# Kernel optimization log

Measured on AMD Instinct MI355X. Metric: run time of the kernel, lower is better.

## Reference

```python
import jax, jax.numpy as jnp
import numpy as np

N = 100_000      # nodes
F_IN = 512       # input feature dim
HID = 8          # hidden per head (layer 1)
HEADS = 8        # heads layer 1
CLS = 7          # num classes (layer 2 out, 1 head)
E = 1_600_000    # random edges (self-loops added in reference)
NEG_SLOPE = 0.2  # PyG GATConv default leaky_relu slope


def setup_inputs() -> dict:
    key = jax.random.key(0)
    ks = jax.random.split(key, 10)
    s1 = 1.0 / np.sqrt(F_IN)
    s2 = 1.0 / np.sqrt(HID * HEADS)
    return {
        "x": jax.random.normal(ks[0], (N, F_IN), jnp.float32),
        "edge_index": jax.random.randint(ks[1], (2, E), 0, N, dtype=jnp.int32),
        "W1": jax.random.normal(ks[2], (F_IN, HEADS * HID), jnp.float32) * s1,
        "a_src1": jax.random.normal(ks[3], (HEADS, HID), jnp.float32) * s1,
        "a_dst1": jax.random.normal(ks[4], (HEADS, HID), jnp.float32) * s1,
        "b1": jnp.zeros((HEADS * HID,), jnp.float32),
        "W2": jax.random.normal(ks[5], (HEADS * HID, CLS), jnp.float32) * s2,
        "a_src2": jax.random.normal(ks[6], (1, CLS), jnp.float32) * s2,
        "a_dst2": jax.random.normal(ks[7], (1, CLS), jnp.float32) * s2,
        "b2": jnp.zeros((CLS,), jnp.float32),
    }


def gat_layer(x, edge_index, W, a_src, a_dst, bias, concat):
    """PyG GATConv (eval mode): linear -> per-edge LeakyReLU score -> edge-softmax over
    incoming edges per dst node -> weighted scatter-sum of src messages."""
    n = x.shape[0]
    H, C = a_src.shape
    h = (x @ W).reshape(n, H, C)                      # [N, H, C]
    src, dst = edge_index[0], edge_index[1]
    alpha_src = (h * a_src).sum(-1)                   # [N, H]
    alpha_dst = (h * a_dst).sum(-1)                   # [N, H]
    e = jax.nn.leaky_relu(alpha_src[src] + alpha_dst[dst], NEG_SLOPE)  # [E, H]
    # numerically stable segment softmax over edges grouped by dst
    m = jax.ops.segment_max(e, dst, num_segments=n)   # [N, H]
    p = jnp.exp(e - m[dst])                           # [E, H]
    denom = jax.ops.segment_sum(p, dst, num_segments=n)
    alpha = p / denom[dst]                            # [E, H]
    out = jax.ops.segment_sum(alpha[:, :, None] * h[src], dst, num_segments=n)  # [N, H, C]
    out = out.reshape(n, H * C) if concat else out.mean(axis=1)
    return out + bias


def reference(x, edge_index, W1, a_src1, a_dst1, b1, W2, a_src2, a_dst2, b2):
    # add self-loops (GATConv default add_self_loops=True)
    loops = jnp.arange(N, dtype=edge_index.dtype)
    ei = jnp.concatenate([edge_index, jnp.stack([loops, loops])], axis=1)
    h = jax.nn.elu(gat_layer(x, ei, W1, a_src1, a_dst1, b1, concat=True))
    out = gat_layer(h, ei, W2, a_src2, a_dst2, b2, concat=False)
    return jax.nn.log_softmax(out, axis=1)
```

## Files before the change

kernel.cpp:

```cpp
#include <hip/hip_runtime.h>
#include <hip/hip_bf16.h>

#define NEG_SLOPE 0.2f
#define SB 256
#define HWG 384

typedef __attribute__((ext_vector_type(8))) short bfrag;
typedef __attribute__((ext_vector_type(4))) float f32x4;
typedef unsigned short ushort_t;

__device__ __forceinline__ float lrelu(float x) {
    return x >= 0.0f ? x : NEG_SLOPE * x;
}
__device__ __forceinline__ unsigned short f2bf(float f) {
    unsigned int u = __float_as_uint(f);
    u += 0x7fffu + ((u >> 16) & 1u);
    return (unsigned short)(u >> 16);
}
__device__ __forceinline__ float bf2f(unsigned short h) {
    return __uint_as_float(((unsigned int)h) << 16);
}
__device__ __forceinline__ float u2lo(unsigned int u) {
    return __uint_as_float(u << 16);
}
__device__ __forceinline__ float u2hi(unsigned int u) {
    return __uint_as_float(u & 0xffff0000u);
}

__global__ __launch_bounds__(256) void hist_prep_kernel(
    const int* __restrict__ edst, int* __restrict__ bcnt, int E, int NB,
    const float* __restrict__ W1, ushort_t* __restrict__ Whi,
    ushort_t* __restrict__ Wlo) {
    if (blockIdx.x < 128) {
        int t = blockIdx.x * 256 + threadIdx.x;
        int k = t >> 6, c = t & 63;
        float w = W1[t];
        unsigned short hi = f2bf(w);
        float rem = w - bf2f(hi);
        int dst = (k >> 7) * 8192 + c * 128 + (k & 127);
        Whi[dst] = hi;
        Wlo[dst] = f2bf(rem);
        return;
    }
    __shared__ int hist[512];
    int tid = threadIdx.x;
    for (int i = tid; i < NB; i += 256) hist[i] = 0;
    __syncthreads();
    int wg = blockIdx.x - 128;
    int CH = (E + HWG - 1) / HWG;
    int st = wg * CH, en = min(st + CH, E);
    for (int i = st + tid; i < en; i += 256)
        atomicAdd(&hist[edst[i] >> 8], 1);
    __syncthreads();
    for (int i = tid; i < NB; i += 256)
        if (hist[i] > 0) atomicAdd(&bcnt[i], hist[i]);
}

__global__ __launch_bounds__(512) void bscan_kernel(
    const int* __restrict__ bcnt, int* __restrict__ boff, int* __restrict__ bcur,
    int* __restrict__ csr_off, int NB, int N, int E) {
    __shared__ int s[512];
    int t = threadIdx.x;
    int v = (t < NB) ? bcnt[t] : 0;
    s[t] = v;
    __syncthreads();
    for (int off = 1; off < 512; off <<= 1) {
        int tv = (t >= off) ? s[t - off] : 0;
        __syncthreads();
        s[t] += tv;
        __syncthreads();
    }
    if (t < NB) {
        int o = s[t] - v;
        boff[t] = o;
        bcur[t] = o;
    }
    if (t == 0) {
        boff[NB] = E;
        csr_off[N] = E;
    }
}

__global__ __launch_bounds__(256) void gemm_bscatter_kernel(
    const float* __restrict__ x, const ushort_t* __restrict__ Whi,
    const ushort_t* __restrict__ Wlo, ushort_t* __restrict__ h1b, int n,
    const int* __restrict__ esrc, const int* __restrict__ edst,
    int* __restrict__ bcur, int2* __restrict__ ebuf, int E, int NB) {
    __shared__ __align__(16) ushort_t Bhi[64 * 136];
    __shared__ __align__(16) ushort_t Blo[64 * 136];
    const int tid = threadIdx.x;

    if (blockIdx.x < SB) {
        int* hist = (int*)Bhi;
        int* base = hist + 512;
        int* rank = hist + 1024;
        for (int i = tid; i < NB; i += 256) { hist[i] = 0; rank[i] = 0; }
        __syncthreads();
        int CH = (E + SB - 1) / SB;
        int st = blockIdx.x * CH, en = min(st + CH, E);
        for (int i = st + tid; i < en; i += 256)
            atomicAdd(&hist[edst[i] >> 8], 1);
        __syncthreads();
        for (int b = tid; b < NB; b += 256)
            if (hist[b] > 0) base[b] = atomicAdd(&bcur[b], hist[b]);
        __syncthreads();
        for (int i = st + tid; i < en; i += 256) {
            int d = edst[i], s = esrc[i];
            int b = d >> 8;
            int r = atomicAdd(&rank[b], 1);
            ebuf[base[b] + r] = make_int2(s, d);
        }
        return;
    }

    const int lane = tid & 63;
    const int wave = tid >> 6;
    const int l15 = lane & 15;
    const int lq = lane >> 4;
    const int wb = (blockIdx.x - SB) * 64 + wave * 16;

    f32x4 acc[4];
    #pragma unroll
    for (int t = 0; t < 4; t++) acc[t] = (f32x4){0.f, 0.f, 0.f, 0.f};

    const int arow = min(wb + l15, n - 1);
    const float* xr = x + (size_t)arow * 512;

    for (int p = 0; p < 4; p++) {
        __syncthreads();
        const ushort_t* sh = Whi + p * 8192;
        const ushort_t* sl = Wlo + p * 8192;
        #pragma unroll
        for (int i = 0; i < 4; i++) {
            int lin = (tid + i * 256) * 8;
            int c = lin >> 7, kk = lin & 127;
            *(bfrag*)&Bhi[c * 136 + kk] = *(const bfrag*)&sh[lin];
            *(bfrag*)&Blo[c * 136 + kk] = *(const bfrag*)&sl[lin];
        }
        __syncthreads();

        #pragma unroll
        for (int step = 0; step < 4; step++) {
            int kb = p * 128 + step * 32 + lq * 8;
            float4 v0 = *(const float4*)&xr[kb];
            float4 v1 = *(const float4*)&xr[kb + 4];
            float xf[8] = {v0.x, v0.y, v0.z, v0.w, v1.x, v1.y, v1.z, v1.w};
            bfrag ah, al;
            #pragma unroll
            for (int j = 0; j < 8; j++) {
                unsigned short hi = f2bf(xf[j]);
                float rem = xf[j] - bf2f(hi);
                ah[j] = (short)hi;
                al[j] = (short)f2bf(rem);
            }
            int kloc = step * 32 + lq * 8;
            #pragma unroll
            for (int t = 0; t < 4; t++) {
                int nrow = t * 16 + l15;
                bfrag bh = *(const bfrag*)&Bhi[nrow * 136 + kloc];
                bfrag bl = *(const bfrag*)&Blo[nrow * 136 + kloc];
                acc[t] = __builtin_amdgcn_mfma_f32_16x16x32_bf16(al, bh, acc[t], 0, 0, 0);
                acc[t] = __builtin_amdgcn_mfma_f32_16x16x32_bf16(ah, bl, acc[t], 0, 0, 0);
                acc[t] = __builtin_amdgcn_mfma_f32_16x16x32_bf16(ah, bh, acc[t], 0, 0, 0);
            }
        }
    }
    #pragma unroll
    for (int t = 0; t < 4; t++) {
        #pragma unroll
        for (int reg = 0; reg < 4; reg++) {
            int grow = wb + lq * 4 + reg;
            if (grow < n) h1b[(size_t)grow * 64 + t * 16 + l15] = f2bf(acc[t][reg]);
        }
    }
}

__global__ __launch_bounds__(256) void finalize_as_kernel(
    const int* __restrict__ boff, const int2* __restrict__ ebuf,
    int* __restrict__ csr_off, int* __restrict__ col, int N, int NB,
    const ushort_t* __restrict__ h1b, const float* __restrict__ a_src1,
    const float* __restrict__ a_dst1, float* __restrict__ as1,
    float* __restrict__ ad1) {
    int tid = threadIdx.x;
    if ((int)blockIdx.x < NB) {
        int b = blockIdx.x;
        __shared__ int cnt[256];
        __shared__ int cur[256];
        __shared__ int sc[256];
        cnt[tid] = 0;
        __syncthreads();
        int st = boff[b], en = boff[b + 1];
        for (int i = st + tid; i < en; i += 256)
            atomicAdd(&cnt[ebuf[i].y & 255], 1);
        __syncthreads();
        int v = cnt[tid];
        sc[tid] = v;
        __syncthreads();
        for (int off = 1; off < 256; off <<= 1) {
            int tv = (tid >= off) ? sc[tid - off] : 0;
            __syncthreads();
            sc[tid] += tv;
            __syncthreads();
        }
        int dbase = b << 8;
        int nd = min(256, N - dbase);
        int o = st + sc[tid] - v;
        if (tid < nd) {
            csr_off[dbase + tid] = o;
            cur[tid] = o;
        }
        __syncthreads();
        for (int i = st + tid; i < en; i += 256) {
            int2 p = ebuf[i];
            int r = atomicAdd(&cur[p.y & 255], 1);
            col[r] = p.x;
        }
        return;
    }
    int idx = ((int)blockIdx.x - NB) * 256 + tid;
    if (idx >= N * 8) return;
    int h = idx & 7;
    const ushort_t* row = h1b + (size_t)(idx >> 3) * 64;
    bfrag hv = *(const bfrag*)&row[h * 8];
    float s = 0.f, d = 0.f;
    #pragma unroll
    for (int j = 0; j < 8; j++) {
        float f = bf2f((unsigned short)hv[j]);
        s = fmaf(f, a_src1[h * 8 + j], s);
        d = fmaf(f, a_dst1[h * 8 + j], d);
    }
    as1[idx] = s;
    ad1[idx] = d;
}

__global__ __launch_bounds__(256) void agg1_kernel(
    const int* __restrict__ csr_off, const int* __restrict__ col,
    const ushort_t* __restrict__ h1b, const float* __restrict__ as1,
    const float* __restrict__ ad1,
    const float* __restrict__ b1, const float* __restrict__ W2,
    const float* __restrict__ a_src2, const float* __restrict__ a_dst2,
    float* __restrict__ g2, float* __restrict__ ad2, int n) {
    int d = blockIdx.x * 8 + (threadIdx.x >> 5);
    if (d >= n) return;
    int c = threadIdx.x & 31;
    int hd = c >> 2;
    const ushort_t* myrow = h1b + (size_t)d * 64;
    float adh = ad1[d * 8 + hd];
    float asd = as1[d * 8 + hd];
    float p0 = __expf(lrelu(asd + adh));
    unsigned int u = *(const unsigned int*)(myrow + c * 2);
    float denom = p0;
    float acc0 = p0 * u2lo(u);
    float acc1 = p0 * u2hi(u);
    int st = csr_off[d], en = csr_off[d + 1];
    int e = st;
    for (; e + 2 <= en; e += 2) {
        int s0 = col[e], s1 = col[e + 1];
        const ushort_t* r0 = h1b + (size_t)s0 * 64;
        const ushort_t* r1 = h1b + (size_t)s1 * 64;
        float a0 = as1[s0 * 8 + hd];
        float a1 = as1[s1 * 8 + hd];
        unsigned int u0 = *(const unsigned int*)(r0 + c * 2);
        unsigned int u1 = *(const unsigned int*)(r1 + c * 2);
        float q0 = __expf(lrelu(a0 + adh));
        float q1 = __expf(lrelu(a1 + adh));
        denom += q0 + q1;
        acc0 = fmaf(q0, u2lo(u0), acc0);
        acc1 = fmaf(q0, u2hi(u0), acc1);
        acc0 = fmaf(q1, u2lo(u1), acc0);
        acc1 = fmaf(q1, u2hi(u1), acc1);
    }
    if (e < en) {
        int s0 = col[e];
        const ushort_t* r0 = h1b + (size_t)s0 * 64;
        float a0 = as1[s0 * 8 + hd];
        unsigned int u0 = *(const unsigned int*)(r0 + c * 2);
        float q0 = __expf(lrelu(a0 + adh));
        denom += q0;
        acc0 = fmaf(q0, u2lo(u0), acc0);
        acc1 = fmaf(q0, u2hi(u0), acc1);
    }
    float v0 = acc0 / denom + b1[2 * c];
    float v1 = acc1 / denom + b1[2 * c + 1];
    float h0 = v0 > 0.f ? v0 : (__expf(v0) - 1.f);
    float h1v = v1 > 0.f ? v1 : (__expf(v1) - 1.f);
    float g[7];
    #pragma unroll
    for (int j = 0; j < 7; j++) {
        float t = fmaf(h0, W2[(2 * c) * 7 + j], h1v * W2[(2 * c + 1) * 7 + j]);
        #pragma unroll
        for (int off = 1; off < 32; off <<= 1) t += __shfl_xor(t, off);
        g[j] = t;
    }
    float sa = 0.f, da = 0.f;
    #pragma unroll
    for (int j = 0; j < 7; j++) {
        sa = fmaf(g[j], a_src2[j], sa);
        da = fmaf(g[j], a_dst2[j], da);
    }
    if (c < 7) g2[(size_t)d * 8 + c] = g[c];
    if (c == 7) g2[(size_t)d * 8 + 7] = sa;
    if (c == 8) ad2[d] = da;
}

__global__ __launch_bounds__(256) void agg2_kernel(
    const int* __restrict__ csr_off, const int* __restrict__ col,
    const float* __restrict__ ad2, const float* __restrict__ g2,
    const float* __restrict__ b2, float* __restrict__ out, int n) {
    int d = blockIdx.x * 4 + (threadIdx.x >> 6);
    if (d >= n) return;
    int lane = threadIdx.x & 63;
    int j = lane >> 3, cc = lane & 7;
    int bl = lane | 7;
    float adv = ad2[d];
    float vd = g2[(size_t)d * 8 + cc];
    float as2d = __shfl(vd, bl);
    float pd = (j == 0) ? __expf(lrelu(as2d + adv)) : 0.f;
    float denom = pd;
    float acc = pd * vd;
    int st = csr_off[d], en = csr_off[d + 1];
    for (int base = st; base < en; base += 8) {
        int eidx = base + j;
        bool valid = eidx < en;
        int s = valid ? col[eidx] : d;
        float val = g2[(size_t)s * 8 + cc];
        float as2s = __shfl(val, bl);
        float p = valid ? __expf(lrelu(as2s + adv)) : 0.f;
        denom += p;
        acc = fmaf(p, val, acc);
    }
    #pragma unroll
    for (int off = 8; off < 64; off <<= 1) {
        acc += __shfl_xor(acc, off);
        denom += __shfl_xor(denom, off);
    }
    float o = acc / denom + ((cc < 7) ? b2[cc] : 0.f);
    float m = (cc < 7) ? o : -1e30f;
    #pragma unroll
    for (int off = 1; off < 8; off <<= 1) m = fmaxf(m, __shfl_xor(m, off));
    float se = (cc < 7) ? __expf(o - m) : 0.f;
    #pragma unroll
    for (int off = 1; off < 8; off <<= 1) se += __shfl_xor(se, off);
    float lse = m + __logf(se);
    if (j == 0 && cc < 7) out[(size_t)d * 7 + cc] = o - lse;
}

extern "C" void kernel_launch(void* const* d_in, const int* in_sizes, int n_in,
                              void* d_out, int out_size, void* d_ws, size_t ws_size,
                              hipStream_t stream) {
    const float* x      = (const float*)d_in[0];
    const int*   ei     = (const int*)d_in[1];
    const float* W1     = (const float*)d_in[2];
    const float* a_src1 = (const float*)d_in[3];
    const float* a_dst1 = (const float*)d_in[4];
    const float* b1     = (const float*)d_in[5];
    const float* W2     = (const float*)d_in[6];
    const float* a_src2 = (const float*)d_in[7];
    const float* a_dst2 = (const float*)d_in[8];
    const float* b2     = (const float*)d_in[9];

    int N = in_sizes[0] / 512;
    int E = in_sizes[1] / 2;
    const int* esrc = ei;
    const int* edst = ei + E;
    int NB = (N + 255) >> 8;

    char* ws = (char*)d_ws;
    size_t off = 0;
    auto alloc = [&](size_t bytes) -> void* {
        void* p = ws + off;
        off += (bytes + 255) & ~(size_t)255;
        return p;
    };
    ushort_t* h1b  = (ushort_t*)alloc((size_t)N * 64 * 2);
    float* as1     = (float*)alloc((size_t)N * 8 * 4);
    float* ad1     = (float*)alloc((size_t)N * 8 * 4);
    float* g2      = (float*)alloc((size_t)N * 8 * 4);
    float* ad2     = (float*)alloc((size_t)N * 4);
    int*   csr_off = (int*)alloc((size_t)(N + 1) * 4);
    int*   col     = (int*)alloc((size_t)E * 4);
    int2*  ebuf    = (int2*)alloc((size_t)E * 8);
    ushort_t* Whi  = (ushort_t*)alloc(512 * 64 * 2);
    ushort_t* Wlo  = (ushort_t*)alloc(512 * 64 * 2);
    int*   bcnt    = (int*)alloc((size_t)NB * 4);
    int*   boff    = (int*)alloc((size_t)(NB + 1) * 4);
    int*   bcur    = (int*)alloc((size_t)NB * 4);

    hipMemsetAsync(bcnt, 0, (size_t)NB * 4, stream);

    int gbl = (N + 63) / 64;
    int abl = (N * 8 + 255) / 256;

    hist_prep_kernel<<<128 + HWG, 256, 0, stream>>>(edst, bcnt, E, NB, W1, Whi, Wlo);
    bscan_kernel<<<1, 512, 0, stream>>>(bcnt, boff, bcur, csr_off, NB, N, E);
    gemm_bscatter_kernel<<<SB + gbl, 256, 0, stream>>>(x, Whi, Wlo, h1b, N,
                                                       esrc, edst, bcur, ebuf, E, NB);
    finalize_as_kernel<<<NB + abl, 256, 0, stream>>>(boff, ebuf, csr_off, col, N, NB,
                                                     h1b, a_src1, a_dst1, as1, ad1);
    agg1_kernel<<<(N + 7) / 8, 256, 0, stream>>>(csr_off, col, h1b, as1, ad1, b1,
                                                 W2, a_src2, a_dst2, g2, ad2, N);
    agg2_kernel<<<(N + 3) / 4, 256, 0, stream>>>(csr_off, col, ad2, g2, b2,
                                                 (float*)d_out, N);
}
```

Before: 479.8 us.

## Fuse attention score projection into GEMM epilogue and unroll agg1 edge loop by four

Computes the per-head alpha_src/alpha_dst dot products directly from the fp32 MFMA accumulators in the GEMM epilogue, using cross-lane shuffles. This removes the separate pass that re-read h1b from memory in the finalize kernel, which now only builds the CSR. The scores now come from fp32 accumulators instead of bf16-rounded values, which changes numerics slightly. The agg1 neighbour loop is also unrolled from 2 to 4 edges so more gather loads are in flight at once, at the cost of extra registers.

```diff
diff --git a/kernel.cpp b/kernel.cpp
--- a/kernel.cpp
+++ b/kernel.cpp
@@ -85,7 +85,9 @@
     const float* __restrict__ x, const ushort_t* __restrict__ Whi,
     const ushort_t* __restrict__ Wlo, ushort_t* __restrict__ h1b, int n,
     const int* __restrict__ esrc, const int* __restrict__ edst,
-    int* __restrict__ bcur, int2* __restrict__ ebuf, int E, int NB) {
+    int* __restrict__ bcur, int2* __restrict__ ebuf, int E, int NB,
+    const float* __restrict__ a_src1, const float* __restrict__ a_dst1,
+    float* __restrict__ as1, float* __restrict__ ad1) {
     __shared__ __align__(16) ushort_t Bhi[64 * 136];
     __shared__ __align__(16) ushort_t Blo[64 * 136];
     const int tid = threadIdx.x;
@@ -173,64 +175,77 @@
             if (grow < n) h1b[(size_t)grow * 64 + t * 16 + l15] = f2bf(acc[t][reg]);
         }
     }
-}
-
-__global__ __launch_bounds__(256) void finalize_as_kernel(
+    const int j7 = l15 & 7;
+    const int wrow = wb + lq * 4 + (j7 & 3);
+    #pragma unroll
+    for (int t = 0; t < 4; t++) {
+        int cidx = t * 16 + l15;
+        float cs = a_src1[cidx];
+        float cd = a_dst1[cidx];
+        float ps0 = acc[t][0] * cs, ps1 = acc[t][1] * cs;
+        float ps2 = acc[t][2] * cs, ps3 = acc[t][3] * cs;
+        float pd0 = acc[t][0] * cd, pd1 = acc[t][1] * cd;
+        float pd2 = acc[t][2] * cd, pd3 = acc[t][3] * cd;
+        #pragma unroll
+        for (int off = 1; off < 8; off <<= 1) {
+            ps0 += __shfl_xor(ps0, off);
+            ps1 += __shfl_xor(ps1, off);
+            ps2 += __shfl_xor(ps2, off);
+            ps3 += __shfl_xor(ps3, off);
+            pd0 += __shfl_xor(pd0, off);
+            pd1 += __shfl_xor(pd1, off);
+            pd2 += __shfl_xor(pd2, off);
+            pd3 += __shfl_xor(pd3, off);
+        }
+        int h = (t << 1) | (l15 >> 3);
+        if (wrow < n) {
+            if (j7 < 4) {
+                float sv = j7 == 0 ? ps0 : j7 == 1 ? ps1 : j7 == 2 ? ps2 : ps3;
+                as1[wrow * 8 + h] = sv;
+            } else {
+                float dv = j7 == 4 ? pd0 : j7 == 5 ? pd1 : j7 == 6 ? pd2 : pd3;
+                ad1[wrow * 8 + h] = dv;
+            }
+        }
+    }
+}
+
+__global__ __launch_bounds__(256) void finalize_kernel(
     const int* __restrict__ boff, const int2* __restrict__ ebuf,
-    int* __restrict__ csr_off, int* __restrict__ col, int N, int NB,
-    const ushort_t* __restrict__ h1b, const float* __restrict__ a_src1,
-    const float* __restrict__ a_dst1, float* __restrict__ as1,
-    float* __restrict__ ad1) {
+    int* __restrict__ csr_off, int* __restrict__ col, int N, int NB) {
     int tid = threadIdx.x;
-    if ((int)blockIdx.x < NB) {
-        int b = blockIdx.x;
-        __shared__ int cnt[256];
-        __shared__ int cur[256];
-        __shared__ int sc[256];
-        cnt[tid] = 0;
-        __syncthreads();
-        int st = boff[b], en = boff[b + 1];
-        for (int i = st + tid; i < en; i += 256)
-            atomicAdd(&cnt[ebuf[i].y & 255], 1);
-        __syncthreads();
-        int v = cnt[tid];
-        sc[tid] = v;
-        __syncthreads();
-        for (int off = 1; off < 256; off <<= 1) {
-            int tv = (tid >= off) ? sc[tid - off] : 0;
-            __syncthreads();
-            sc[tid] += tv;
-            __syncthreads();
-        }
-        int dbase = b << 8;
-        int nd = min(256, N - dbase);
-        int o = st + sc[tid] - v;
-        if (tid < nd) {
-            csr_off[dbase + tid] = o;
-            cur[tid] = o;
-        }
-        __syncthreads();
-        for (int i = st + tid; i < en; i += 256) {
-            int2 p = ebuf[i];
-            int r = atomicAdd(&cur[p.y & 255], 1);
-            col[r] = p.x;
-        }
-        return;
-    }
-    int idx = ((int)blockIdx.x - NB) * 256 + tid;
-    if (idx >= N * 8) return;
-    int h = idx & 7;
-    const ushort_t* row = h1b + (size_t)(idx >> 3) * 64;
-    bfrag hv = *(const bfrag*)&row[h * 8];
-    float s = 0.f, d = 0.f;
-    #pragma unroll
-    for (int j = 0; j < 8; j++) {
-        float f = bf2f((unsigned short)hv[j]);
-        s = fmaf(f, a_src1[h * 8 + j], s);
-        d = fmaf(f, a_dst1[h * 8 + j], d);
-    }
-    as1[idx] = s;
-    ad1[idx] = d;
+    int b = blockIdx.x;
+    __shared__ int cnt[256];
+    __shared__ int cur[256];
+    __shared__ int sc[256];
+    cnt[tid] = 0;
+    __syncthreads();
+    int st = boff[b], en = boff[b + 1];
+    for (int i = st + tid; i < en; i += 256)
+        atomicAdd(&cnt[ebuf[i].y & 255], 1);
+    __syncthreads();
+    int v = cnt[tid];
+    sc[tid] = v;
+    __syncthreads();
+    for (int off = 1; off < 256; off <<= 1) {
+        int tv = (tid >= off) ? sc[tid - off] : 0;
+        __syncthreads();
+        sc[tid] += tv;
+        __syncthreads();
+    }
+    int dbase = b << 8;
+    int nd = min(256, N - dbase);
+    int o = st + sc[tid] - v;
+    if (tid < nd) {
+        csr_off[dbase + tid] = o;
+        cur[tid] = o;
+    }
+    __syncthreads();
+    for (int i = st + tid; i < en; i += 256) {
+        int2 p = ebuf[i];
+        int r = atomicAdd(&cur[p.y & 255], 1);
+        col[r] = p.x;
+    }
 }
 
 __global__ __launch_bounds__(256) void agg1_kernel(
@@ -254,23 +269,35 @@
     float acc1 = p0 * u2hi(u);
     int st = csr_off[d], en = csr_off[d + 1];
     int e = st;
-    for (; e + 2 <= en; e += 2) {
-        int s0 = col[e], s1 = col[e + 1];
+    for (; e + 4 <= en; e += 4) {
+        int s0 = col[e], s1 = col[e + 1], s2 = col[e + 2], s3 = col[e + 3];
         const ushort_t* r0 = h1b + (size_t)s0 * 64;
         const ushort_t* r1 = h1b + (size_t)s1 * 64;
+        const ushort_t* r2 = h1b + (size_t)s2 * 64;
+        const ushort_t* r3 = h1b + (size_t)s3 * 64;
         float a0 = as1[s0 * 8 + hd];
         float a1 = as1[s1 * 8 + hd];
+        float a2 = as1[s2 * 8 + hd];
+        float a3 = as1[s3 * 8 + hd];
         unsigned int u0 = *(const unsigned int*)(r0 + c * 2);
         unsigned int u1 = *(const unsigned int*)(r1 + c * 2);
+        unsigned int u2 = *(const unsigned int*)(r2 + c * 2);
+        unsigned int u3 = *(const unsigned int*)(r3 + c * 2);
         float q0 = __expf(lrelu(a0 + adh));
         float q1 = __expf(lrelu(a1 + adh));
-        denom += q0 + q1;
+        float q2 = __expf(lrelu(a2 + adh));
+        float q3 = __expf(lrelu(a3 + adh));
+        denom += (q0 + q1) + (q2 + q3);
         acc0 = fmaf(q0, u2lo(u0), acc0);
         acc1 = fmaf(q0, u2hi(u0), acc1);
         acc0 = fmaf(q1, u2lo(u1), acc0);
         acc1 = fmaf(q1, u2hi(u1), acc1);
-    }
-    if (e < en) {
+        acc0 = fmaf(q2, u2lo(u2), acc0);
+        acc1 = fmaf(q2, u2hi(u2), acc1);
+        acc0 = fmaf(q3, u2lo(u3), acc0);
+        acc1 = fmaf(q3, u2hi(u3), acc1);
+    }
+    for (; e < en; ++e) {
         int s0 = col[e];
         const ushort_t* r0 = h1b + (size_t)s0 * 64;
         float a0 = as1[s0 * 8 + hd];
@@ -389,14 +416,13 @@
     hipMemsetAsync(bcnt, 0, (size_t)NB * 4, stream);
 
     int gbl = (N + 63) / 64;
-    int abl = (N * 8 + 255) / 256;
 
     hist_prep_kernel<<<128 + HWG, 256, 0, stream>>>(edst, bcnt, E, NB, W1, Whi, Wlo);
     bscan_kernel<<<1, 512, 0, stream>>>(bcnt, boff, bcur, csr_off, NB, N, E);
     gemm_bscatter_kernel<<<SB + gbl, 256, 0, stream>>>(x, Whi, Wlo, h1b, N,
-                                                       esrc, edst, bcur, ebuf, E, NB);
-    finalize_as_kernel<<<NB + abl, 256, 0, stream>>>(boff, ebuf, csr_off, col, N, NB,
-                                                     h1b, a_src1, a_dst1, as1, ad1);
+                                                       esrc, edst, bcur, ebuf, E, NB,
+                                                       a_src1, a_dst1, as1, ad1);
+    finalize_kernel<<<NB, 256, 0, stream>>>(boff, ebuf, csr_off, col, N, NB);
     agg1_kernel<<<(N + 7) / 8, 256, 0, stream>>>(csr_off, col, h1b, as1, ad1, b1,
                                                  W2, a_src2, a_dst2, g2, ad2, N);
     agg2_kernel<<<(N + 3) / 4, 256, 0, stream>>>(csr_off, col, ad2, g2, b2,
```

New measurement: 472.9 us. About the same (-1.4%).
